# Performance work log

Hardware: AMD Instinct MI355X
Metric: run time of the kernel (lower is better)

The kernel has to match this reference:

```python
import jax, jax.numpy as jnp
import numpy as np

B, T, C, H, HS = 2, 2048, 1024, 16, 64


def setup_inputs() -> dict:
    key = jax.random.key(0)
    ks = jax.random.split(key, 7)
    x = jax.random.normal(ks[0], (B, T, C), dtype=jnp.float32)
    # causal mask, broadcast over batch (True = attend)
    attention_mask = jnp.broadcast_to(jnp.tril(jnp.ones((T, T), dtype=bool)), (B, T, T))
    s = 1.0 / np.sqrt(C)
    wq = jax.random.normal(ks[1], (H, C, HS), dtype=jnp.float32) * s   # per-head query Linear (no bias)
    wk = jax.random.normal(ks[2], (H, C, HS), dtype=jnp.float32) * s
    wv = jax.random.normal(ks[3], (H, C, HS), dtype=jnp.float32) * s
    wproj = jax.random.normal(ks[4], (H * HS, C), dtype=jnp.float32) * (1.0 / np.sqrt(H * HS))
    bproj = jnp.zeros((C,), dtype=jnp.float32)
    return {"x": x, "attention_mask": attention_mask,
            "wq": wq, "wk": wk, "wv": wv, "wproj": wproj, "bproj": bproj}


def reference(x, attention_mask, wq, wk, wv, wproj, bproj):
    # per-head projections: [B,H,T,HS]
    q = jnp.einsum('btc,hcd->bhtd', x, wq)
    k = jnp.einsum('btc,hcd->bhtd', x, wk)
    v = jnp.einsum('btc,hcd->bhtd', x, wv)
    scale = 1.0 / jnp.sqrt(jnp.asarray(HS, dtype=x.dtype))
    wei = jnp.einsum('bhtd,bhsd->bhts', q, k) * scale          # [B,H,T,T]
    wei = jnp.where(attention_mask[:, None, :, :], wei, -jnp.inf)
    wei = jax.nn.softmax(wei, axis=-1)
    out = jnp.einsum('bhts,bhsd->bhtd', wei, v)                 # [B,H,T,HS]
    out = out.transpose(0, 2, 1, 3).reshape(B, T, H * HS)       # concat heads
    return out @ wproj + bproj                                  # [B,T,C]
```

## Files before the change

kernel.cpp:

```cpp
#include <hip/hip_runtime.h>
#include <math.h>

typedef float f32x4 __attribute__((ext_vector_type(4)));
typedef __bf16 bf16x8 __attribute__((ext_vector_type(8)));
typedef unsigned short u16x8 __attribute__((ext_vector_type(8)));
typedef unsigned short u16x4 __attribute__((ext_vector_type(4)));

#define DEV static __device__ __forceinline__

DEV unsigned short f2bf(float f) {
    unsigned int u = __builtin_bit_cast(unsigned int, f);
    u += 0x7fffu + ((u >> 16) & 1u);
    return (unsigned short)(u >> 16);
}

#define GLD16(gp, lp) __builtin_amdgcn_global_load_lds( \
    (__attribute__((address_space(1))) void*)(gp),      \
    (__attribute__((address_space(3))) void*)(lp), 16, 0, 0)

#define WAITBAR(N) asm volatile("s_waitcnt vmcnt(" #N ")\n\ts_barrier" ::: "memory")
#define BARRIER()  asm volatile("s_barrier" ::: "memory")

__global__ __launch_bounds__(256) void k_prep(const float* __restrict__ x,
                                              const float* __restrict__ wq,
                                              const float* __restrict__ wk,
                                              const float* __restrict__ wv,
                                              const float* __restrict__ wproj,
                                              unsigned short* __restrict__ xb,
                                              unsigned short* __restrict__ WqkvT,
                                              unsigned short* __restrict__ WprojT) {
    const int bid = blockIdx.x, tid = threadIdx.x;
    if (bid < 2048) {
        int i = bid * 256 + tid;
        const float4* p = (const float4*)(x + (size_t)i * 8);
        float4 a = p[0], b = p[1];
        u16x8 o;
        o[0] = f2bf(a.x); o[1] = f2bf(a.y); o[2] = f2bf(a.z); o[3] = f2bf(a.w);
        o[4] = f2bf(b.x); o[5] = f2bf(b.y); o[6] = f2bf(b.z); o[7] = f2bf(b.w);
        *(u16x8*)(xb + (size_t)i * 8) = o;
        return;
    }
    __shared__ unsigned short t[64][68];
    if (bid < 2816) {
        int zb = bid - 2048;
        int z = zb >> 4, wsel = z >> 4, zz = z & 15;
        const float* src = (wsel == 0 ? wq : wsel == 1 ? wk : wv) + (size_t)zz * 65536;
        int r0 = (zb & 15) * 64;
#pragma unroll
        for (int it = 0; it < 4; ++it) {
            int r = (tid >> 4) + it * 16;
            int c4 = (tid & 15) * 4;
            float4 v = *(const float4*)&src[(size_t)(r0 + r) * 64 + c4];
            t[c4 + 0][r] = f2bf(v.x);
            t[c4 + 1][r] = f2bf(v.y);
            t[c4 + 2][r] = f2bf(v.z);
            t[c4 + 3][r] = f2bf(v.w);
        }
        __syncthreads();
#pragma unroll
        for (int it = 0; it < 4; ++it) {
            int c = (tid >> 4) + it * 16;
            int r4 = (tid & 15) * 4;
            u16x4 o;
            o[0] = t[c][r4 + 0]; o[1] = t[c][r4 + 1];
            o[2] = t[c][r4 + 2]; o[3] = t[c][r4 + 3];
            int row = wsel * 1024 + zz * 64 + c;
            *(u16x4*)&WqkvT[(size_t)row * 1024 + r0 + r4] = o;
        }
    } else {
        int zb = bid - 2816;
        int r0 = (zb & 15) * 64, c0 = (zb >> 4) * 64;
#pragma unroll
        for (int it = 0; it < 4; ++it) {
            int r = (tid >> 4) + it * 16;
            int c4 = (tid & 15) * 4;
            float4 v = *(const float4*)&wproj[(size_t)(r0 + r) * 1024 + c0 + c4];
            t[c4 + 0][r] = f2bf(v.x);
            t[c4 + 1][r] = f2bf(v.y);
            t[c4 + 2][r] = f2bf(v.z);
            t[c4 + 3][r] = f2bf(v.w);
        }
        __syncthreads();
#pragma unroll
        for (int it = 0; it < 4; ++it) {
            int c = (tid >> 4) + it * 16;
            int r4 = (tid & 15) * 4;
            u16x4 o;
            o[0] = t[c][r4 + 0]; o[1] = t[c][r4 + 1];
            o[2] = t[c][r4 + 2]; o[3] = t[c][r4 + 3];
            *(u16x4*)&WprojT[(size_t)(c0 + c) * 1024 + r0 + r4] = o;
        }
    }
}

template <int STAGE, int M_REP, int NB, int SUPM, int SUPN>
__global__ __launch_bounds__(256) void k_gemm(const unsigned short* __restrict__ A,
                                              const unsigned short* __restrict__ Bt,
                                              int Kd,
                                              float* __restrict__ outF,
                                              const float* __restrict__ bias,
                                              unsigned short* __restrict__ Qb,
                                              unsigned short* __restrict__ Kb,
                                              unsigned short* __restrict__ Vt) {
    constexpr int BM = M_REP * 32;
    __shared__ unsigned short As[2][BM * 64] __attribute__((aligned(16)));
    __shared__ unsigned short Bs[2][128 * 64] __attribute__((aligned(16)));
    const int tid = threadIdx.x, l = tid & 63, w = tid >> 6;
    constexpr int BN_CH = NB / SUPN;
    const int orig = blockIdx.x;
    const int xcd = orig & 7, sdx = orig >> 3;
    const int bm = (xcd / BN_CH) * SUPM + (sdx % SUPM);
    const int bn = (xcd % BN_CH) * SUPN + (sdx / SUPM);
    const int wr = w >> 1, wc = w & 1;
    const int g = l >> 4, q = l & 15;
    f32x4 acc[M_REP][4] = {};
    const int lr = l >> 3, lc = (l & 7) ^ lr;
    const unsigned short* gA = A + (size_t)(bm * BM + w * 8 + lr) * Kd + lc * 8;
    const unsigned short* gB = Bt + (size_t)(bn * 128 + w * 8 + lr) * Kd + lc * 8;

#define GSTAGE(buf, k0) do {                                                  \
        _Pragma("unroll")                                                     \
        for (int it = 0; it < M_REP; ++it)                                    \
            GLD16(gA + (size_t)(it * 32) * Kd + (k0), &As[buf][(it * 32 + w * 8) * 64]); \
        _Pragma("unroll")                                                     \
        for (int it = 0; it < 4; ++it)                                        \
            GLD16(gB + (size_t)(it * 32) * Kd + (k0), &Bs[buf][(it * 32 + w * 8) * 64]); \
    } while (0)

    const int nt = Kd >> 6;
    GSTAGE(0, 0);
    int cur = 0;
    for (int t = 0; t < nt; ++t) {
        if (t + 1 < nt) {
            GSTAGE(cur ^ 1, (t + 1) << 6);
            if constexpr (M_REP == 4) WAITBAR(8); else WAITBAR(6);
        } else {
            WAITBAR(0);
        }
#pragma unroll
        for (int ks = 0; ks < 2; ++ks) {
            bf16x8 af[M_REP], bfr[4];
#pragma unroll
            for (int mi = 0; mi < M_REP; ++mi) {
                int ra = wr * (M_REP * 16) + mi * 16 + q;
                af[mi] = *(const bf16x8*)&As[cur][ra * 64 + (((ks * 4 + g) ^ (q & 7)) * 8)];
            }
#pragma unroll
            for (int ni = 0; ni < 4; ++ni) {
                int rb = wc * 64 + ni * 16 + q;
                bfr[ni] = *(const bf16x8*)&Bs[cur][rb * 64 + (((ks * 4 + g) ^ (q & 7)) * 8)];
            }
#pragma unroll
            for (int mi = 0; mi < M_REP; ++mi)
#pragma unroll
                for (int ni = 0; ni < 4; ++ni)
                    acc[mi][ni] = __builtin_amdgcn_mfma_f32_16x16x32_bf16(
                        af[mi], bfr[ni], acc[mi][ni], 0, 0, 0);
        }
        BARRIER();
        cur ^= 1;
    }
#undef GSTAGE
#pragma unroll
    for (int mi = 0; mi < M_REP; ++mi)
#pragma unroll
        for (int ni = 0; ni < 4; ++ni)
#pragma unroll
            for (int r = 0; r < 4; ++r) {
                float c = acc[mi][ni][r];
                int m = bm * BM + wr * (M_REP * 16) + mi * 16 + g * 4 + r;
                int n = bn * 128 + wc * 64 + ni * 16 + q;
                if (STAGE == 1) {
                    int b = m >> 11, t = m & 2047;
                    int proj = n >> 10, rr = n & 1023, h = rr >> 6, d = rr & 63;
                    int bh = b * 16 + h;
                    if (proj == 0)
                        Qb[((size_t)bh * 2048 + t) * 64 + d] = f2bf(c * 0.18033688011112042f);
                    else if (proj == 1)
                        Kb[((size_t)bh * 2048 + t) * 64 + d] = f2bf(c);
                    else
                        Vt[((size_t)bh * 64 + d) * 2048 + t] = f2bf(c);
                } else {
                    outF[(size_t)m * 1024 + n] = c + bias[n];
                }
            }
}

__global__ __launch_bounds__(256) void k_attn(const unsigned short* __restrict__ Qb,
                                              const unsigned short* __restrict__ Kb,
                                              const unsigned short* __restrict__ Vt,
                                              unsigned short* __restrict__ att) {
    __shared__ unsigned short Ks[2][2][4096] __attribute__((aligned(16)));
    __shared__ unsigned short Vs[2][2][4096] __attribute__((aligned(16)));
    __shared__ unsigned short P[4][16][72];
    const int tid = threadIdx.x, l = tid & 63, w = tid >> 6;
    const int pj = blockIdx.x, bh = blockIdx.y;
    const int b = bh >> 4, h = bh & 15;
    const int ql = l & 15, g = l >> 4;
    const unsigned short* Qp = Qb + (size_t)bh * 2048 * 64;
    const unsigned short* Kp = Kb + (size_t)bh * 2048 * 64;
    const unsigned short* Vp = Vt + (size_t)bh * 64 * 2048;

    const int sr0 = w * 16 + (l >> 3);
    const int sch = (l & 7) ^ (l >> 3);
    const unsigned short* gK0 = Kp + (size_t)sr0 * 64 + sch * 8;
    const unsigned short* gK1 = gK0 + 8 * 64;
    const unsigned short* gV0 = Vp + (size_t)sr0 * 2048 + sch * 8;
    const unsigned short* gV1 = gV0 + 8 * 2048;

#define ATT_STAGE(buf, kvb) do {                                                  \
        GLD16(gK0 + (size_t)(kvb) * 64, &Ks[buf][0][(w * 16) * 64]);              \
        GLD16(gK1 + (size_t)(kvb) * 64, &Ks[buf][0][(w * 16 + 8) * 64]);          \
        GLD16(gK0 + (size_t)((kvb) + 64) * 64, &Ks[buf][1][(w * 16) * 64]);       \
        GLD16(gK1 + (size_t)((kvb) + 64) * 64, &Ks[buf][1][(w * 16 + 8) * 64]);   \
        GLD16(gV0 + (kvb), &Vs[buf][0][(w * 16) * 64]);                           \
        GLD16(gV1 + (kvb), &Vs[buf][0][(w * 16 + 8) * 64]);                       \
        GLD16(gV0 + (kvb) + 64, &Vs[buf][1][(w * 16) * 64]);                      \
        GLD16(gV1 + (kvb) + 64, &Vs[buf][1][(w * 16 + 8) * 64]);                  \
    } while (0)

    for (int ph = 0; ph < 2; ++ph) {
        const int qt = ph ? (31 - pj) : pj;
        const int qg = qt * 64 + w * 16 + ql;
        const int minqg = qt * 64 + w * 16;
        const int nkv2 = (qt + 2) >> 1;

        bf16x8 qf0 = *(const bf16x8*)(Qp + (size_t)qg * 64 + g * 8);
        bf16x8 qf1 = *(const bf16x8*)(Qp + (size_t)qg * 64 + 32 + g * 8);
        f32x4 ot[4] = {};
        float mrun = -1e30f, lsum = 0.f;

        ATT_STAGE(0, 0);
        int cur = 0;

        for (int kb = 0; kb < nkv2; ++kb) {
            if (kb + 1 < nkv2) {
                ATT_STAGE(cur ^ 1, (kb + 1) * 128);
                WAITBAR(8);
            } else {
                WAITBAR(0);
            }
#pragma unroll
            for (int sub = 0; sub < 2; ++sub) {
                const int kvb = kb * 128 + sub * 64;
                const unsigned short* Kt = &Ks[cur][sub][0];
                const unsigned short* Vtl = &Vs[cur][sub][0];
                f32x4 st[4] = {};
                bf16x8 kf0[4], kf1[4];
#pragma unroll
                for (int f = 0; f < 4; ++f) {
                    int rk = f * 16 + ql, sw = rk & 7;
                    kf0[f] = *(const bf16x8*)&Kt[rk * 64 + ((g ^ sw) * 8)];
                    kf1[f] = *(const bf16x8*)&Kt[rk * 64 + (((g + 4) ^ sw) * 8)];
                }
                __builtin_amdgcn_s_setprio(1);
#pragma unroll
                for (int f = 0; f < 4; ++f) {
                    st[f] = __builtin_amdgcn_mfma_f32_16x16x32_bf16(kf0[f], qf0, st[f], 0, 0, 0);
                    st[f] = __builtin_amdgcn_mfma_f32_16x16x32_bf16(kf1[f], qf1, st[f], 0, 0, 0);
                }
                __builtin_amdgcn_s_setprio(0);
                if (kvb + 63 > minqg) {
#pragma unroll
                    for (int f = 0; f < 4; ++f)
#pragma unroll
                        for (int r = 0; r < 4; ++r)
                            if (kvb + f * 16 + g * 4 + r > qg) st[f][r] = -1e30f;
                }
                float pmax = -1e30f;
#pragma unroll
                for (int f = 0; f < 4; ++f)
#pragma unroll
                    for (int r = 0; r < 4; ++r) pmax = fmaxf(pmax, st[f][r]);
                if (!__all(pmax <= mrun + 8.f)) {
                    float pm = fmaxf(pmax, __shfl_xor(pmax, 16));
                    pm = fmaxf(pm, __shfl_xor(pm, 32));
                    float mnew = fmaxf(mrun, pm);
                    float corr = __builtin_amdgcn_exp2f(mrun - mnew);
                    lsum *= corr;
#pragma unroll
                    for (int f = 0; f < 4; ++f) ot[f] *= corr;
                    mrun = mnew;
                }
                float psum = 0.f;
#pragma unroll
                for (int f = 0; f < 4; ++f) {
                    u16x4 pk;
#pragma unroll
                    for (int r = 0; r < 4; ++r) {
                        float p = __builtin_amdgcn_exp2f(st[f][r] - mrun);
                        psum += p;
                        pk[r] = f2bf(p);
                    }
                    *(u16x4*)&P[w][ql][f * 16 + g * 4] = pk;
                }
                lsum += psum;
                asm volatile("s_waitcnt lgkmcnt(0)" ::: "memory");
#pragma unroll
                for (int dc = 0; dc < 2; ++dc) {
                    bf16x8 pf = *(const bf16x8*)&P[w][ql][dc * 32 + g * 8];
                    __builtin_amdgcn_s_setprio(1);
#pragma unroll
                    for (int f = 0; f < 4; ++f) {
                        int rv = f * 16 + ql, sw = rv & 7;
                        bf16x8 vf = *(const bf16x8*)&Vtl[rv * 64 + (((dc * 4 + g) ^ sw) * 8)];
                        ot[f] = __builtin_amdgcn_mfma_f32_16x16x32_bf16(vf, pf, ot[f], 0, 0, 0);
                    }
                    __builtin_amdgcn_s_setprio(0);
                }
            }
            BARRIER();
            cur ^= 1;
        }
        lsum += __shfl_xor(lsum, 16);
        lsum += __shfl_xor(lsum, 32);
        float inv = 1.f / lsum;
        unsigned short* ap = att + ((size_t)(b * 2048 + qg)) * 1024 + h * 64;
#pragma unroll
        for (int f = 0; f < 4; ++f) {
            u16x4 o;
#pragma unroll
            for (int r = 0; r < 4; ++r) o[r] = f2bf(ot[f][r] * inv);
            *(u16x4*)&ap[f * 16 + g * 4] = o;
        }
    }
#undef ATT_STAGE
}

extern "C" void kernel_launch(void* const* d_in, const int* in_sizes, int n_in,
                              void* d_out, int out_size, void* d_ws, size_t ws_size,
                              hipStream_t stream) {
    const float* x = (const float*)d_in[0];
    const float* wq = (const float*)d_in[2];
    const float* wk = (const float*)d_in[3];
    const float* wv = (const float*)d_in[4];
    const float* wproj = (const float*)d_in[5];
    const float* bproj = (const float*)d_in[6];
    float* out = (float*)d_out;

    char* ws = (char*)d_ws;
    unsigned short* xb     = (unsigned short*)(ws);
    unsigned short* WqkvT  = (unsigned short*)(ws + (8u << 20));
    unsigned short* WprojT = (unsigned short*)(ws + (14u << 20));
    unsigned short* Qb     = (unsigned short*)(ws + (16u << 20));
    unsigned short* Kb     = (unsigned short*)(ws + (24u << 20));
    unsigned short* Vt     = (unsigned short*)(ws + (32u << 20));
    unsigned short* att    = xb;

    k_prep<<<3072, 256, 0, stream>>>(x, wq, wk, wv, wproj, xb, WqkvT, WprojT);
    k_gemm<1, 4, 24, 8, 12><<<768, 256, 0, stream>>>(xb, WqkvT, 1024, nullptr, nullptr, Qb, Kb, Vt);
    k_attn<<<dim3(16, 32), 256, 0, stream>>>(Qb, Kb, Vt, att);
    k_gemm<3, 2, 8, 16, 4><<<512, 256, 0, stream>>>(att, WprojT, 1024, out, bproj, nullptr, nullptr, nullptr);
}
```

Baseline: 124.0 us.

## Restructure M_REP==4 GEMM mainloop to prefetch two K-tiles ahead

For the M_REP==4 GEMM variant, the loop now preloads two K-tiles before it starts. Each iteration reads both k-substeps' fragments into registers first, then issues the global-to-LDS load for tile t+2 into the buffer just consumed, between two barriers, before running the last MFMA batch. The goal is to hide global load latency more deeply and overlap the next copy with MFMA work. The cost is an extra barrier per iteration and higher register pressure from holding both fragment sets. The M_REP==2 path is unchanged.

```diff
diff --git a/kernel.cpp b/kernel.cpp
--- a/kernel.cpp
+++ b/kernel.cpp
@@ -128,37 +128,94 @@
     } while (0)
 
     const int nt = Kd >> 6;
-    GSTAGE(0, 0);
-    int cur = 0;
-    for (int t = 0; t < nt; ++t) {
-        if (t + 1 < nt) {
-            GSTAGE(cur ^ 1, (t + 1) << 6);
-            if constexpr (M_REP == 4) WAITBAR(8); else WAITBAR(6);
-        } else {
-            WAITBAR(0);
-        }
-#pragma unroll
-        for (int ks = 0; ks < 2; ++ks) {
-            bf16x8 af[M_REP], bfr[4];
-#pragma unroll
-            for (int mi = 0; mi < M_REP; ++mi) {
-                int ra = wr * (M_REP * 16) + mi * 16 + q;
-                af[mi] = *(const bf16x8*)&As[cur][ra * 64 + (((ks * 4 + g) ^ (q & 7)) * 8)];
-            }
-#pragma unroll
-            for (int ni = 0; ni < 4; ++ni) {
-                int rb = wc * 64 + ni * 16 + q;
-                bfr[ni] = *(const bf16x8*)&Bs[cur][rb * 64 + (((ks * 4 + g) ^ (q & 7)) * 8)];
-            }
-#pragma unroll
-            for (int mi = 0; mi < M_REP; ++mi)
-#pragma unroll
-                for (int ni = 0; ni < 4; ++ni)
-                    acc[mi][ni] = __builtin_amdgcn_mfma_f32_16x16x32_bf16(
-                        af[mi], bfr[ni], acc[mi][ni], 0, 0, 0);
-        }
+    if constexpr (M_REP == 4) {
+        GSTAGE(0, 0);
+        GSTAGE(1, 64);
+        asm volatile("s_waitcnt vmcnt(8)" ::: "memory");
         BARRIER();
-        cur ^= 1;
+        for (int t = 0; t < nt; ++t) {
+            const int cur = t & 1;
+            {
+                bf16x8 af[4], bfr[4];
+#pragma unroll
+                for (int mi = 0; mi < 4; ++mi) {
+                    int ra = wr * 64 + mi * 16 + q;
+                    af[mi] = *(const bf16x8*)&As[cur][ra * 64 + ((g ^ (q & 7)) * 8)];
+                }
+#pragma unroll
+                for (int ni = 0; ni < 4; ++ni) {
+                    int rb = wc * 64 + ni * 16 + q;
+                    bfr[ni] = *(const bf16x8*)&Bs[cur][rb * 64 + ((g ^ (q & 7)) * 8)];
+                }
+#pragma unroll
+                for (int mi = 0; mi < 4; ++mi)
+#pragma unroll
+                    for (int ni = 0; ni < 4; ++ni)
+                        acc[mi][ni] = __builtin_amdgcn_mfma_f32_16x16x32_bf16(
+                            af[mi], bfr[ni], acc[mi][ni], 0, 0, 0);
+            }
+            {
+                bf16x8 af[4], bfr[4];
+#pragma unroll
+                for (int mi = 0; mi < 4; ++mi) {
+                    int ra = wr * 64 + mi * 16 + q;
+                    af[mi] = *(const bf16x8*)&As[cur][ra * 64 + (((4 + g) ^ (q & 7)) * 8)];
+                }
+#pragma unroll
+                for (int ni = 0; ni < 4; ++ni) {
+                    int rb = wc * 64 + ni * 16 + q;
+                    bfr[ni] = *(const bf16x8*)&Bs[cur][rb * 64 + (((4 + g) ^ (q & 7)) * 8)];
+                }
+                asm volatile("s_waitcnt lgkmcnt(0)" ::: "memory");
+                BARRIER();
+                if (t + 2 < nt) {
+                    GSTAGE(cur, (t + 2) << 6);
+                    asm volatile("s_waitcnt vmcnt(8)" ::: "memory");
+                } else {
+                    asm volatile("s_waitcnt vmcnt(0)" ::: "memory");
+                }
+                BARRIER();
+#pragma unroll
+                for (int mi = 0; mi < 4; ++mi)
+#pragma unroll
+                    for (int ni = 0; ni < 4; ++ni)
+                        acc[mi][ni] = __builtin_amdgcn_mfma_f32_16x16x32_bf16(
+                            af[mi], bfr[ni], acc[mi][ni], 0, 0, 0);
+            }
+        }
+    } else {
+        GSTAGE(0, 0);
+        int cur = 0;
+        for (int t = 0; t < nt; ++t) {
+            if (t + 1 < nt) {
+                GSTAGE(cur ^ 1, (t + 1) << 6);
+                WAITBAR(6);
+            } else {
+                WAITBAR(0);
+            }
+#pragma unroll
+            for (int ks = 0; ks < 2; ++ks) {
+                bf16x8 af[M_REP], bfr[4];
+#pragma unroll
+                for (int mi = 0; mi < M_REP; ++mi) {
+                    int ra = wr * (M_REP * 16) + mi * 16 + q;
+                    af[mi] = *(const bf16x8*)&As[cur][ra * 64 + (((ks * 4 + g) ^ (q & 7)) * 8)];
+                }
+#pragma unroll
+                for (int ni = 0; ni < 4; ++ni) {
+                    int rb = wc * 64 + ni * 16 + q;
+                    bfr[ni] = *(const bf16x8*)&Bs[cur][rb * 64 + (((ks * 4 + g) ^ (q & 7)) * 8)];
+                }
+#pragma unroll
+                for (int mi = 0; mi < M_REP; ++mi)
+#pragma unroll
+                    for (int ni = 0; ni < 4; ++ni)
+                        acc[mi][ni] = __builtin_amdgcn_mfma_f32_16x16x32_bf16(
+                            af[mi], bfr[ni], acc[mi][ni], 0, 0, 0);
+            }
+            BARRIER();
+            cur ^= 1;
+        }
     }
 #undef GSTAGE
 #pragma unroll
```

After: 125.7 us. Within noise of the previous version (+1.4%).
